# Kernel optimization log

Hardware: AMD Instinct MI355X
Metric: run time of the kernel (lower is better)

The kernel has to match this reference:

```python
import jax, jax.numpy as jnp
from jax import lax
import numpy as np

B, C_IN, H, W = 4, 64, 192, 192
NPT = 128          # num_point
MAXC = 32          # objects per image
INIT_STRIDE, COARSE_STRIDE, DOWN = 10.0, 4.0, 4.0


def setup_inputs() -> dict:
    key = jax.random.key(0)
    ks = jax.random.split(key, 8)
    wh_pred = jax.random.normal(ks[0], (B, 2 * NPT, H, W), jnp.float32)
    cnn_feature = jax.random.normal(ks[1], (B, C_IN, H, W), jnp.float32)
    conv1_w = jax.random.normal(ks[2], (256, C_IN, 3, 3), jnp.float32) * 0.05
    conv1_b = jnp.zeros((256,), jnp.float32)
    conv2_w = jax.random.normal(ks[3], (C_IN, 256, 1, 1), jnp.float32) * 0.05
    conv2_b = jnp.zeros((C_IN,), jnp.float32)
    w_poly = jax.random.normal(ks[4], (NPT * 4, (NPT + 1) * C_IN), jnp.float32) * 0.02
    w_fuse = jax.random.normal(ks[5], (NPT * 2, NPT * 4), jnp.float32) * 0.02
    b_fuse = jnp.zeros((NPT * 2,), jnp.float32)
    ct_ind = jax.random.randint(ks[6], (B, MAXC), 0, H * W, jnp.int32)
    ct_img_idx = jnp.repeat(jnp.arange(B, dtype=jnp.int32), MAXC).reshape(B, MAXC)
    ct_num = jnp.full((B,), MAXC, jnp.int32)
    return {"wh_pred": wh_pred, "cnn_feature": cnn_feature,
            "conv1_w": conv1_w, "conv1_b": conv1_b, "conv2_w": conv2_w, "conv2_b": conv2_b,
            "w_poly": w_poly, "w_fuse": w_fuse, "b_fuse": b_fuse,
            "ct_ind": ct_ind, "ct_img_idx": ct_img_idx, "ct_num": ct_num}


def _conv(x, w, b, pad):
    y = lax.conv_general_dilated(x, w, (1, 1), [(pad, pad), (pad, pad)],
                                 dimension_numbers=("NCHW", "OIHW", "NCHW"))
    return y + b[None, :, None, None]


def _pnp(polys, h, w):
    # even-odd ray-casting rasterization: polys [N,P,2] (x,y) -> masks [N,h,w]
    N, P, _ = polys.shape
    yy = jnp.arange(h, dtype=polys.dtype)[None, :, None]   # [1,h,1]
    xx = jnp.arange(w, dtype=polys.dtype)[None, None, :]   # [1,1,w]
    v2 = jnp.roll(polys, -1, axis=1)
    edges = (polys[:, :, 0].T, polys[:, :, 1].T, v2[:, :, 0].T, v2[:, :, 1].T)  # each [P,N]

    def step(par, e):
        x1, y1, x2, y2 = [a[:, None, None] for a in e]      # [N,1,1]
        cond = (y1 > yy) != (y2 > yy)
        den = y2 - y1
        den = jnp.where(jnp.abs(den) < 1e-9, 1e-9, den)
        xint = x1 + (x2 - x1) * (yy - y1) / den
        return jnp.logical_xor(par, cond & (xx < xint)), None

    par0 = jnp.zeros((N, h, w), dtype=bool)
    par, _ = lax.scan(step, par0, edges)
    return par.astype(polys.dtype)


def _mask_batch(mask, ct_num, bs, h, w):
    # faithful to original buggy scatter: offset uses ct_num[i-1], not a cumulative sum
    cn = [int(v) for v in np.asarray(ct_num)]
    mc = max(cn)
    mb = jnp.zeros((bs, mc, h, w), mask.dtype)
    mb = mb.at[0, :cn[0]].set(mask[:cn[0]])
    for i in range(1, bs):
        mb = mb.at[i, :cn[i]].set(mask[cn[i - 1]:cn[i - 1] + cn[i]])
    return mb


def _sample(feat, pts, img_idx):
    # bilinear grid_sample (align_corners=False, zero padding): feat [B,C,H,W], pts [N,P,2] pixel coords
    Bf, C, Hf, Wf = feat.shape
    x = pts[..., 0] - 0.5
    y = pts[..., 1] - 0.5
    x0f = jnp.floor(x); y0f = jnp.floor(y)
    wx = (x - x0f)[..., None]; wy = (y - y0f)[..., None]
    x0 = x0f.astype(jnp.int32); y0 = y0f.astype(jnp.int32)

    def g(xi, yi):
        valid = (xi >= 0) & (xi < Wf) & (yi >= 0) & (yi < Hf)
        v = feat[img_idx[:, None], :, jnp.clip(yi, 0, Hf - 1), jnp.clip(xi, 0, Wf - 1)]  # [N,P,C]
        return v * valid[..., None]

    out = (g(x0, y0) * (1 - wx) * (1 - wy) + g(x0 + 1, y0) * wx * (1 - wy)
           + g(x0, y0 + 1) * (1 - wx) * wy + g(x0 + 1, y0 + 1) * wx * wy)
    return jnp.transpose(out, (0, 2, 1))  # [N,C,P]


def _decode(wh_pred, cnn_feature, conv1_w, conv1_b, conv2_w, conv2_b,
            w_poly, w_fuse, b_fuse, ct_ind, ct_img_idx, ct_num):
    bs, _, h, w = cnn_feature.shape
    ind = ct_ind.reshape(-1)        # ct_01 assumed all valid
    img = ct_img_idx.reshape(-1)
    cx = ind % w
    cy = ind // w
    off = wh_pred[img, :, cy, cx].reshape(ind.shape[0], -1, 2)   # [N, num_point, 2]
    ct = jnp.stack([cx, cy], axis=1).astype(wh_pred.dtype)       # [N,2]
    init_polys = off * INIT_STRIDE + ct[:, None, :]

    # Refine_wtih_pnp.trans_feature
    t = jax.nn.relu(_conv(cnn_feature, conv1_w, conv1_b, 1))
    feat = _conv(t, conv2_w, conv2_b, 0)

    # PnP_contour_feature (init)
    m_init = _pnp(init_polys, h, w)
    mb_init = _mask_batch(m_init, ct_num, bs, h, w)
    feat = jax.nn.relu(jnp.max(mb_init, axis=1, keepdims=True) * feat + feat)

    # GCN-style point feature sampling + global deform
    pts = jnp.concatenate([ct[:, None, :], init_polys], axis=1)  # [N, P+1, 2]
    fp = _sample(feat, pts, img).reshape(ind.shape[0], -1)       # [N, C*(P+1)]
    offsets = ((fp @ w_poly.T) @ w_fuse.T + b_fuse).reshape(-1, NPT, 2)
    coarse = offsets * COARSE_STRIDE + lax.stop_gradient(init_polys)

    # coarse_pnp
    m_c = _pnp(coarse, h, w)
    mb_c = _mask_batch(m_c, ct_num, bs, h, w)
    feat = jax.nn.relu(jnp.max(mb_c, axis=1, keepdims=True) * feat + feat)

    return init_polys * DOWN, coarse * DOWN, mb_init, mb_c, feat


def reference(wh_pred, cnn_feature, conv1_w, conv1_b, conv2_w, conv2_b,
              w_poly, w_fuse, b_fuse, ct_ind, ct_img_idx, ct_num):
    return _decode(wh_pred, cnn_feature, conv1_w, conv1_b, conv2_w, conv2_b,
                   w_poly, w_fuse, b_fuse, ct_ind, ct_img_idx, ct_num)
```

## Files before the change

kernel.cpp:

```cpp
#include <hip/hip_runtime.h>
#include <hip/hip_bf16.h>

#define HH 192
#define WW 192
#define HW 36864
#define CHW 2359296

typedef __attribute__((ext_vector_type(8))) short short8;
typedef __attribute__((ext_vector_type(4))) float float4v;

static __device__ __forceinline__ unsigned short f2bu(float f) {
  union { float f; unsigned u; } v; v.f = f;
  unsigned r = (v.u + 0x7fffu + ((v.u >> 16) & 1u)) >> 16;
  return (unsigned short)r;
}

static __device__ __forceinline__ float bu2f(unsigned short s) {
  union { unsigned u; float f; } v; v.u = ((unsigned)s) << 16;
  return v.f;
}

__global__ void k_prep(const float* __restrict__ c1w, const float* __restrict__ c2w,
                       const float* __restrict__ wfuse,
                       unsigned short* __restrict__ wB1, unsigned short* __restrict__ wB2,
                       float* __restrict__ wfT, float* __restrict__ tmp,
                       float* __restrict__ u01) {
  int i = blockIdx.x * 256 + threadIdx.x;
  if (i < 147456) {
    int T = i / 9216, r = i % 9216;
    int s = r / 512, e = r % 512;
    int l = e >> 3, j = e & 7;
    int m = l & 15, q = l >> 4;
    int oc = T * 16 + m;
    int k = s * 32 + q * 8 + j;
    int tap = k >> 6, ic = k & 63;
    int ky = tap / 3, kx = tap % 3;
    wB1[i] = f2bu(c1w[((oc * 64 + ic) * 3 + ky) * 3 + kx]);
    return;
  }
  int j2 = i - 147456;
  if (j2 < 16384) {
    int g = j2 / 512, e = j2 % 512;
    int l = e >> 3, jj = e & 7;
    int m = l & 15, q = l >> 4;
    int w = g / 8, s2 = g % 8;
    wB2[j2] = f2bu(c2w[(w * 16 + m) * 256 + s2 * 32 + q * 8 + jj]);
    return;
  }
  int k3 = j2 - 16384;
  if (k3 < 131072) { int jj = k3 >> 8, r = k3 & 255; wfT[k3] = wfuse[r * 512 + jj]; return; }
  int z = k3 - 131072;
  if (z < 65536) { tmp[z] = 0.f; return; }
  int v = z - 65536;
  if (v < 294912) u01[v] = 0.f;
}

__global__ void k_init_polys(const float* __restrict__ wh, const int* __restrict__ ct_ind,
                             const int* __restrict__ ct_img,
                             float* __restrict__ initp, float* __restrict__ out0) {
  int n = blockIdx.x;
  int p = threadIdx.x;
  int ind = ct_ind[n], img = ct_img[n];
  int cx = ind % WW, cy = ind / WW;
  size_t base = ((size_t)(img * 256 + 2 * p)) * HW + (size_t)cy * WW + cx;
  float ox = wh[base];
  float oy = wh[base + HW];
  float px = __fadd_rn(__fmul_rn(ox, 10.0f), (float)cx);
  float py = __fadd_rn(__fmul_rn(oy, 10.0f), (float)cy);
  initp[n * 256 + 2 * p]     = px;
  initp[n * 256 + 2 * p + 1] = py;
  out0[n * 256 + 2 * p]      = __fmul_rn(px, 4.0f);
  out0[n * 256 + 2 * p + 1]  = __fmul_rn(py, 4.0f);
}

__global__ __launch_bounds__(256, 2) void k_conv(const float* __restrict__ x,
    const unsigned short* __restrict__ wB1, const float* __restrict__ b1,
    const unsigned short* __restrict__ wB2, const float* __restrict__ b2,
    const float* __restrict__ u0, float* __restrict__ feat,
    unsigned short* __restrict__ featT) {
  int blk = blockIdx.x;
  int b    = blk / 288;
  int rem  = blk % 288;
  int pair = rem / 3;
  int xs   = rem % 3;
  int y0 = pair * 2, x0 = xs * 64;
  int t = threadIdx.x;
  int w = t >> 6, l = t & 63;
  int m = l & 15, q = l >> 4;

  __shared__ __align__(16) unsigned short sb[33792];

  for (int it = 0; it < 66; ++it) {
    int idx = it * 256 + t;
    int r  = idx / 4224;
    int r2 = idx - r * 4224;
    int ic = r2 / 66;
    int xx = r2 - ic * 66;
    int gy = y0 + r - 1, gx = x0 + xx - 1;
    float v = 0.f;
    if (gy >= 0 && gy < HH && gx >= 0 && gx < WW)
      v = x[(size_t)(b * 64 + ic) * HW + (size_t)gy * WW + gx];
    sb[(r * 66 + xx) * 72 + ic] = f2bu(v);
  }
  __syncthreads();

  float4v acc1[8][4];
#pragma unroll
  for (int nt = 0; nt < 4; ++nt) {
    float bv = b1[w * 64 + nt * 16 + m];
#pragma unroll
    for (int mt = 0; mt < 8; ++mt) acc1[mt][nt] = (float4v){bv, bv, bv, bv};
  }

#pragma unroll
  for (int s = 0; s < 18; ++s) {
    int tap = s >> 1, ky = tap / 3, kx = tap - ky * 3;
    int ic0 = (s & 1) * 32 + q * 8;
    short8 bF[4];
#pragma unroll
    for (int nt = 0; nt < 4; ++nt)
      bF[nt] = *(const short8*)&wB1[(size_t)((((w * 4 + nt) * 18 + s) * 512) + l * 8)];
    short8 aF[8];
#pragma unroll
    for (int mt = 0; mt < 8; ++mt) {
      int col  = (mt & 3) * 16 + m + kx;
      int rowi = ky + (mt >> 2);
      aF[mt] = *(const short8*)&sb[(rowi * 66 + col) * 72 + ic0];
    }
#pragma unroll
    for (int nt = 0; nt < 4; ++nt)
#pragma unroll
      for (int mt = 0; mt < 8; ++mt)
        acc1[mt][nt] = __builtin_amdgcn_mfma_f32_16x16x32_bf16(aF[mt], bF[nt], acc1[mt][nt], 0, 0, 0);
  }
  __syncthreads();

#pragma unroll
  for (int mt = 0; mt < 8; ++mt)
#pragma unroll
    for (int nt = 0; nt < 4; ++nt)
#pragma unroll
      for (int r = 0; r < 4; ++r) {
        int p = mt * 16 + q * 4 + r;
        int oc = w * 64 + nt * 16 + m;
        sb[p * 264 + oc] = f2bu(fmaxf(acc1[mt][nt][r], 0.f));
      }
  __syncthreads();

  float4v acc2[8];
  {
    float bv = b2[w * 16 + m];
#pragma unroll
    for (int mt = 0; mt < 8; ++mt) acc2[mt] = (float4v){bv, bv, bv, bv};
  }
#pragma unroll
  for (int s2 = 0; s2 < 8; ++s2) {
    short8 bF2 = *(const short8*)&wB2[(size_t)(((w * 8 + s2) * 512) + l * 8)];
#pragma unroll
    for (int mt = 0; mt < 8; ++mt) {
      short8 a2 = *(const short8*)&sb[(mt * 16 + m) * 264 + s2 * 32 + q * 8];
      acc2[mt] = __builtin_amdgcn_mfma_f32_16x16x32_bf16(a2, bF2, acc2[mt], 0, 0, 0);
    }
  }
  __syncthreads();

  float* fS = (float*)sb;
#pragma unroll
  for (int mt = 0; mt < 8; ++mt)
#pragma unroll
    for (int r = 0; r < 4; ++r) {
      int p = mt * 16 + q * 4 + r;
      fS[w * 2112 + m * 132 + p] = acc2[mt][r];
    }
  const float* ub = u0 + b * HW;
#pragma unroll
  for (int i = 0; i < 32; ++i) {
    int idx = i * 64 + l;
    int c16 = idx >> 7, p = idx & 127;
    float f = fS[w * 2112 + c16 * 132 + p];
    int gy = y0 + (p >> 6), gx = x0 + (p & 63);
    float uu = ub[gy * WW + gx];
    feat[(size_t)(b * 64 + w * 16 + c16) * HW + (size_t)gy * WW + gx] = fmaxf(uu * f + f, 0.f);
  }
  {
    unsigned short* ft = featT + (size_t)b * HW * 64;
    int c2 = (l & 7) * 2;
#pragma unroll
    for (int i = 0; i < 16; ++i) {
      int p = (l >> 3) + 8 * i;
      float f0 = fS[w * 2112 + c2 * 132 + p];
      float f1 = fS[w * 2112 + (c2 + 1) * 132 + p];
      int gy = y0 + (p >> 6), gx = x0 + (p & 63);
      float uu = ub[gy * WW + gx];
      f0 = fmaxf(uu * f0 + f0, 0.f);
      f1 = fmaxf(uu * f1 + f1, 0.f);
      unsigned v = (unsigned)f2bu(f0) | ((unsigned)f2bu(f1) << 16);
      *(unsigned*)&ft[((size_t)(gy * WW + gx)) * 64 + w * 16 + c2] = v;
    }
  }
}

__global__ __launch_bounds__(64) void k_pnp(const float* __restrict__ polys,
                                            float* __restrict__ outm,
                                            float* __restrict__ u) {
  int row  = blockIdx.x;
  int n    = blockIdx.y;
  int lane = threadIdx.x;
  __shared__ float vx[128], vy[128], xint[128];
  __shared__ int cnt;
  if (lane == 0) cnt = 0;
  vx[lane]      = polys[n * 256 + 2 * lane];
  vy[lane]      = polys[n * 256 + 2 * lane + 1];
  vx[lane + 64] = polys[n * 256 + 2 * (lane + 64)];
  vy[lane + 64] = polys[n * 256 + 2 * (lane + 64) + 1];
  __syncthreads();
  float yy = (float)row;
  for (int e = lane; e < 128; e += 64) {
    float y1 = vy[e], y2 = vy[(e + 1) & 127];
    if ((y1 > yy) != (y2 > yy)) {
      float x1 = vx[e], x2 = vx[(e + 1) & 127];
      float den = __fsub_rn(y2, y1);
      if (fabsf(den) < 1e-9f) den = 1e-9f;
      float xi = __fadd_rn(x1, __fdiv_rn(__fmul_rn(__fsub_rn(x2, x1), __fsub_rn(yy, y1)), den));
      xint[atomicAdd(&cnt, 1)] = xi;
    }
  }
  __syncthreads();
  int mm = cnt;
  int bb = (n < 32) ? 0 : 1;
  int cc = n & 31;
  size_t base = ((size_t)(bb * 32 + cc) * HH + row) * WW;
  for (int xp = lane; xp < WW; xp += 64) {
    float xf = (float)xp;
    int c = 0;
    for (int j = 0; j < mm; ++j) c += (xf < xint[j]) ? 1 : 0;
    float mv = (float)(c & 1);
    outm[base + xp] = mv;
    if (n >= 32) {
      outm[base + (size_t)32 * HW + xp] = mv;
      outm[base + (size_t)64 * HW + xp] = mv;
    }
    if (c & 1) {
      int off = bb * HW + row * WW + xp;
      atomicOr((int*)(u + off), 0x3f800000);
      if (n >= 32) {
        atomicOr((int*)(u + off + HW), 0x3f800000);
        atomicOr((int*)(u + off + 2 * HW), 0x3f800000);
      }
    }
  }
}

__global__ __launch_bounds__(256) void k_sample(const unsigned short* __restrict__ featT,
    const float* __restrict__ initp, const int* __restrict__ ct_ind,
    const int* __restrict__ ct_img, float* __restrict__ fp) {
  int n  = blockIdx.x;
  int ch = blockIdx.y;
  int t  = threadIdx.x;
  int w  = t >> 6, lane = t & 63;
  int c  = lane & 31;
  int ph = lane >> 5;

  __shared__ float sF[4128];

  int img = ct_img[n];
  int ind = ct_ind[n];
  float ctx = (float)(ind % WW), cty = (float)(ind / WW);
  const unsigned short* fb = featT + (size_t)img * HW * 64 + ch * 32 + c;

  for (int i = 0; i < 17; ++i) {
    int p = i * 8 + w * 2 + ph;
    if (p < 129) {
      float px, py;
      if (p == 0) { px = ctx; py = cty; }
      else {
        px = initp[n * 256 + 2 * (p - 1)];
        py = initp[n * 256 + 2 * (p - 1) + 1];
      }
      float x = __fsub_rn(px, 0.5f), y = __fsub_rn(py, 0.5f);
      float x0f = floorf(x), y0f = floorf(y);
      float wx = __fsub_rn(x, x0f), wy = __fsub_rn(y, y0f);
      int x0 = (int)x0f, y0 = (int)y0f;
      float g[4];
#pragma unroll
      for (int qq = 0; qq < 4; ++qq) {
        int xi = x0 + (qq & 1), yi = y0 + (qq >> 1);
        bool valid = (xi >= 0) && (xi < WW) && (yi >= 0) && (yi < HH);
        int xc = min(max(xi, 0), WW - 1), yc = min(max(yi, 0), HH - 1);
        float v = bu2f(fb[(size_t)(yc * WW + xc) * 64]);
        g[qq] = valid ? v : 0.f;
      }
      float omx = __fsub_rn(1.f, wx), omy = __fsub_rn(1.f, wy);
      float r = __fadd_rn(__fadd_rn(__fadd_rn(
          __fmul_rn(__fmul_rn(g[0], omx), omy),
          __fmul_rn(__fmul_rn(g[1], wx),  omy)),
          __fmul_rn(__fmul_rn(g[2], omx), wy)),
          __fmul_rn(__fmul_rn(g[3], wx),  wy));
      sF[c * 129 + p] = r;
    }
  }
  __syncthreads();
  float* dst = fp + (size_t)n * 8256 + (size_t)ch * 4128;
  for (int idx = t; idx < 4128; idx += 256) dst[idx] = sF[idx];
}

__global__ __launch_bounds__(256) void k_gemm1(const float* __restrict__ fp,
    const float* __restrict__ wpoly, float* __restrict__ tmp) {
  int ntile = blockIdx.x;
  int jtile = blockIdx.y;
  int ks    = blockIdx.z;
  int c0 = (129 * ks) / 32, c1 = (129 * (ks + 1)) / 32;
  int t = threadIdx.x;
  int tn = t & 15, tj = t >> 4;
  __shared__ float aS[64][65];
  __shared__ float bS[64][65];
  float acc[4][4];
#pragma unroll
  for (int i = 0; i < 4; ++i)
#pragma unroll
    for (int j = 0; j < 4; ++j) acc[i][j] = 0.f;
  for (int ch = c0; ch < c1; ++ch) {
    int k0 = ch * 64;
    __syncthreads();
    for (int idx = t; idx < 4096; idx += 256) {
      int r = idx >> 6, cc = idx & 63;
      aS[cc][r] = fp[(size_t)(ntile * 64 + r) * 8256 + k0 + cc];
      bS[cc][r] = wpoly[(size_t)(jtile * 64 + r) * 8256 + k0 + cc];
    }
    __syncthreads();
    for (int kk = 0; kk < 64; ++kk) {
      float a0 = aS[kk][tn * 4], a1 = aS[kk][tn * 4 + 1], a2 = aS[kk][tn * 4 + 2], a3 = aS[kk][tn * 4 + 3];
      float b0 = bS[kk][tj * 4], b1 = bS[kk][tj * 4 + 1], b2 = bS[kk][tj * 4 + 2], b3 = bS[kk][tj * 4 + 3];
      acc[0][0] = fmaf(a0, b0, acc[0][0]); acc[0][1] = fmaf(a0, b1, acc[0][1]);
      acc[0][2] = fmaf(a0, b2, acc[0][2]); acc[0][3] = fmaf(a0, b3, acc[0][3]);
      acc[1][0] = fmaf(a1, b0, acc[1][0]); acc[1][1] = fmaf(a1, b1, acc[1][1]);
      acc[1][2] = fmaf(a1, b2, acc[1][2]); acc[1][3] = fmaf(a1, b3, acc[1][3]);
      acc[2][0] = fmaf(a2, b0, acc[2][0]); acc[2][1] = fmaf(a2, b1, acc[2][1]);
      acc[2][2] = fmaf(a2, b2, acc[2][2]); acc[2][3] = fmaf(a2, b3, acc[2][3]);
      acc[3][0] = fmaf(a3, b0, acc[3][0]); acc[3][1] = fmaf(a3, b1, acc[3][1]);
      acc[3][2] = fmaf(a3, b2, acc[3][2]); acc[3][3] = fmaf(a3, b3, acc[3][3]);
    }
  }
#pragma unroll
  for (int i = 0; i < 4; ++i)
#pragma unroll
    for (int j = 0; j < 4; ++j)
      atomicAdd(&tmp[(size_t)(ntile * 64 + tn * 4 + i) * 512 + jtile * 64 + tj * 4 + j], acc[i][j]);
}

__global__ __launch_bounds__(256) void k_gemm2(const float* __restrict__ tmp,
    const float* __restrict__ wfT, const float* __restrict__ bfuse,
    const float* __restrict__ initp, float* __restrict__ coarse, float* __restrict__ out1) {
  int n = blockIdx.x, r = threadIdx.x;
  __shared__ float tS[512];
  tS[r] = tmp[n * 512 + r];
  tS[r + 256] = tmp[n * 512 + 256 + r];
  __syncthreads();
  float acc = 0.f;
  for (int j = 0; j < 512; ++j) acc = fmaf(wfT[j * 256 + r], tS[j], acc);
  acc = __fadd_rn(acc, bfuse[r]);
  float cr = __fadd_rn(__fmul_rn(acc, 4.0f), initp[n * 256 + r]);
  coarse[n * 256 + r] = cr;
  out1[n * 256 + r] = __fmul_rn(cr, 4.0f);
}

__global__ void k_final(float* __restrict__ feat, const float* __restrict__ u) {
  size_t i = ((size_t)blockIdx.x * 256 + threadIdx.x) * 4;
  int b = (int)(i / ((size_t)CHW));
  int yx = (int)(i % HW);
  float4v f = *(float4v*)&feat[i];
  float4v uu = *(const float4v*)&u[b * HW + yx];
  float4v o;
#pragma unroll
  for (int j = 0; j < 4; ++j) o[j] = fmaxf(__fadd_rn(__fmul_rn(uu[j], f[j]), f[j]), 0.f);
  *(float4v*)&feat[i] = o;
}

extern "C" void kernel_launch(void* const* d_in, const int* in_sizes, int n_in,
                              void* d_out, int out_size, void* d_ws, size_t ws_size,
                              hipStream_t stream) {
  const float* wh    = (const float*)d_in[0];
  const float* cnnf  = (const float*)d_in[1];
  const float* c1w   = (const float*)d_in[2];
  const float* c1b   = (const float*)d_in[3];
  const float* c2w   = (const float*)d_in[4];
  const float* c2b   = (const float*)d_in[5];
  const float* wpoly = (const float*)d_in[6];
  const float* wfuse = (const float*)d_in[7];
  const float* bfuse = (const float*)d_in[8];
  const int* ct_ind  = (const int*)d_in[9];
  const int* ct_img  = (const int*)d_in[10];

  float* ws    = (float*)d_ws;
  float* wfT   = ws;
  float* initp = wfT + 131072;
  float* coarse= initp + 32768;
  float* tmp   = coarse + 32768;
  float* u0    = tmp + 65536;
  float* u1    = u0 + 147456;
  float* fpbuf = u1 + 147456;
  unsigned short* wB1 = (unsigned short*)(fpbuf + 1056768);
  unsigned short* wB2 = wB1 + 147456;

  float* out0 = (float*)d_out;
  float* out1 = out0 + 32768;
  float* out2 = out1 + 32768;
  float* out3 = out2 + 4718592;
  float* out4 = out3 + 4718592;
  float* feat = out4;
  unsigned short* featT = (unsigned short*)out3;

  k_prep<<<2560, 256, 0, stream>>>(c1w, c2w, wfuse, wB1, wB2, wfT, tmp, u0);
  k_init_polys<<<128, 128, 0, stream>>>(wh, ct_ind, ct_img, initp, out0);
  k_pnp<<<dim3(192, 64), 64, 0, stream>>>(initp, out2, u0);
  k_conv<<<1152, 256, 0, stream>>>(cnnf, wB1, c1b, wB2, c2b, u0, feat, featT);
  k_sample<<<dim3(128, 2), 256, 0, stream>>>(featT, initp, ct_ind, ct_img, fpbuf);
  k_gemm1<<<dim3(2, 8, 32), 256, 0, stream>>>(fpbuf, wpoly, tmp);
  k_gemm2<<<128, 256, 0, stream>>>(tmp, wfT, bfuse, initp, coarse, out1);
  k_pnp<<<dim3(192, 64), 64, 0, stream>>>(coarse, out3, u1);
  k_final<<<9216, 256, 0, stream>>>(feat, u1);
}
```

Measured before the change: 503.4 us.

## Shrink conv LDS footprint, vectorize halo load, split second GEMM in halves

The fused conv kernel now stages the relu'd hidden activations into shared memory in two halves of 64 pixels each, running the 1x1 conv per half. This cuts the shared buffer from about 66KB to about 38KB. The input tile load switches to float4 global reads with a separate scalar pass for the two halo columns. Launch bounds are raised to request 4 blocks per CU. This targets higher occupancy and fewer global load instructions, at the cost of an extra barrier and possible register pressure or spills from the 4-block bound with 128 accumulator floats live.

```diff
diff --git a/kernel.cpp b/kernel.cpp
--- a/kernel.cpp
+++ b/kernel.cpp
@@ -73,7 +73,7 @@
   out0[n * 256 + 2 * p + 1]  = __fmul_rn(py, 4.0f);
 }
 
-__global__ __launch_bounds__(256, 2) void k_conv(const float* __restrict__ x,
+__global__ __launch_bounds__(256, 4) void k_conv(const float* __restrict__ x,
     const unsigned short* __restrict__ wB1, const float* __restrict__ b1,
     const unsigned short* __restrict__ wB2, const float* __restrict__ b2,
     const float* __restrict__ u0, float* __restrict__ feat,
@@ -88,19 +88,37 @@
   int w = t >> 6, l = t & 63;
   int m = l & 15, q = l >> 4;
 
-  __shared__ __align__(16) unsigned short sb[33792];
-
-  for (int it = 0; it < 66; ++it) {
-    int idx = it * 256 + t;
-    int r  = idx / 4224;
-    int r2 = idx - r * 4224;
-    int ic = r2 / 66;
-    int xx = r2 - ic * 66;
-    int gy = y0 + r - 1, gx = x0 + xx - 1;
-    float v = 0.f;
-    if (gy >= 0 && gy < HH && gx >= 0 && gx < WW)
-      v = x[(size_t)(b * 64 + ic) * HW + (size_t)gy * WW + gx];
-    sb[(r * 66 + xx) * 72 + ic] = f2bu(v);
+  __shared__ __align__(16) unsigned short sb[19008];
+
+  {
+    int kq = t & 15;
+    int pr = t >> 4;
+    for (int itr = 0; itr < 16; ++itr) {
+      int pi = itr * 16 + pr;
+      int r  = pi >> 6;
+      int ic = pi & 63;
+      int gy = y0 + r - 1;
+      float4v v = (float4v){0.f, 0.f, 0.f, 0.f};
+      if (gy >= 0 && gy < HH)
+        v = *(const float4v*)&x[(size_t)(b * 64 + ic) * HW + (size_t)gy * WW + x0 + kq * 4];
+      int base = (r * 66 + 1 + kq * 4) * 72 + ic;
+      sb[base]       = f2bu(v[0]);
+      sb[base + 72]  = f2bu(v[1]);
+      sb[base + 144] = f2bu(v[2]);
+      sb[base + 216] = f2bu(v[3]);
+    }
+    for (int itr = 0; itr < 2; ++itr) {
+      int e = itr * 256 + t;
+      int xxh = e >> 8;
+      int rm = e & 255;
+      int r = rm >> 6, ic = rm & 63;
+      int gy = y0 + r - 1;
+      int gx = x0 - 1 + xxh * 65;
+      float v = 0.f;
+      if (gy >= 0 && gy < HH && gx >= 0 && gx < WW)
+        v = x[(size_t)(b * 64 + ic) * HW + (size_t)gy * WW + gx];
+      sb[(r * 66 + xxh * 65) * 72 + ic] = f2bu(v);
+    }
   }
   __syncthreads();
 
@@ -136,7 +154,7 @@
   __syncthreads();
 
 #pragma unroll
-  for (int mt = 0; mt < 8; ++mt)
+  for (int mt = 0; mt < 4; ++mt)
 #pragma unroll
     for (int nt = 0; nt < 4; ++nt)
 #pragma unroll
@@ -147,19 +165,48 @@
       }
   __syncthreads();
 
-  float4v acc2[8];
+  float4v acc2a[4];
   {
     float bv = b2[w * 16 + m];
 #pragma unroll
-    for (int mt = 0; mt < 8; ++mt) acc2[mt] = (float4v){bv, bv, bv, bv};
+    for (int mt = 0; mt < 4; ++mt) acc2a[mt] = (float4v){bv, bv, bv, bv};
   }
 #pragma unroll
   for (int s2 = 0; s2 < 8; ++s2) {
     short8 bF2 = *(const short8*)&wB2[(size_t)(((w * 8 + s2) * 512) + l * 8)];
 #pragma unroll
-    for (int mt = 0; mt < 8; ++mt) {
+    for (int mt = 0; mt < 4; ++mt) {
       short8 a2 = *(const short8*)&sb[(mt * 16 + m) * 264 + s2 * 32 + q * 8];
-      acc2[mt] = __builtin_amdgcn_mfma_f32_16x16x32_bf16(a2, bF2, acc2[mt], 0, 0, 0);
+      acc2a[mt] = __builtin_amdgcn_mfma_f32_16x16x32_bf16(a2, bF2, acc2a[mt], 0, 0, 0);
+    }
+  }
+  __syncthreads();
+
+#pragma unroll
+  for (int mt = 4; mt < 8; ++mt)
+#pragma unroll
+    for (int nt = 0; nt < 4; ++nt)
+#pragma unroll
+      for (int r = 0; r < 4; ++r) {
+        int p = mt * 16 + q * 4 + r;
+        int oc = w * 64 + nt * 16 + m;
+        sb[(p - 64) * 264 + oc] = f2bu(fmaxf(acc1[mt][nt][r], 0.f));
+      }
+  __syncthreads();
+
+  float4v acc2b[4];
+  {
+    float bv = b2[w * 16 + m];
+#pragma unroll
+    for (int mt = 0; mt < 4; ++mt) acc2b[mt] = (float4v){bv, bv, bv, bv};
+  }
+#pragma unroll
+  for (int s2 = 0; s2 < 8; ++s2) {
+    short8 bF2 = *(const short8*)&wB2[(size_t)(((w * 8 + s2) * 512) + l * 8)];
+#pragma unroll
+    for (int mt = 0; mt < 4; ++mt) {
+      short8 a2 = *(const short8*)&sb[(mt * 16 + m) * 264 + s2 * 32 + q * 8];
+      acc2b[mt] = __builtin_amdgcn_mfma_f32_16x16x32_bf16(a2, bF2, acc2b[mt], 0, 0, 0);
     }
   }
   __syncthreads();
@@ -170,7 +217,8 @@
 #pragma unroll
     for (int r = 0; r < 4; ++r) {
       int p = mt * 16 + q * 4 + r;
-      fS[w * 2112 + m * 132 + p] = acc2[mt][r];
+      float v = (mt < 4) ? acc2a[mt][r] : acc2b[mt - 4][r];
+      fS[w * 2112 + m * 132 + p] = v;
     }
   const float* ub = u0 + b * HW;
 #pragma unroll
```

New measurement: 874.9 us. 1.74x slower.
